# Optimization experiments

Measured on AMD Instinct MI355X. Metric: run time of the kernel, lower is better.

The kernel has to match this reference:

```python
import jax, jax.numpy as jnp
import numpy as np

B, S, H = 4, 2048, 1024
E, I, K = 8, 2048, 2


def setup_inputs() -> dict:
    key = jax.random.key(0)
    ks = jax.random.split(key, 6)
    return {
        "hidden_states": jax.random.normal(ks[0], (B, S, H), dtype=jnp.float32),
        "Wg": jax.random.normal(ks[1], (H, E), dtype=jnp.float32) * 0.02,
        "W1": jax.random.normal(ks[2], (E, H, I), dtype=jnp.float32) * 0.02,
        "b1": jnp.zeros((E, I), dtype=jnp.float32),
        "W2": jax.random.normal(ks[3], (E, I, H), dtype=jnp.float32) * 0.02,
        "b2": jnp.zeros((E, H), dtype=jnp.float32),
    }


def reference(hidden_states, Wg, W1, b1, W2, b2):
    b, s, h = hidden_states.shape
    x = hidden_states.reshape(-1, h)                      # [T, H]
    gate_logits = x @ Wg                                  # [T, E]
    gate_probs = jax.nn.softmax(gate_logits, axis=-1)
    topk_probs, topk_idx = jax.lax.top_k(gate_probs, K)   # [T, K]
    topk_probs = topk_probs / jnp.sum(topk_probs, axis=-1, keepdims=True)
    # dense combine weights [T, E] (zero where expert not selected)
    T = x.shape[0]
    w = jnp.zeros((T, E), dtype=x.dtype)
    w = w.at[jnp.arange(T)[:, None], topk_idx].set(topk_probs)
    # run every expert on all tokens (dense grouped-GEMM form), exact erf GELU
    h1 = jax.nn.gelu(jnp.einsum('th,ehi->eti', x, W1) + b1[:, None, :], approximate=False)  # [E, T, I]
    y = jnp.einsum('eti,eih->eth', h1, W2) + b2[:, None, :]                                  # [E, T, H]
    out = jnp.einsum('te,eth->th', w, y)                                                     # [T, H]
    return out.reshape(b, s, h)
```

## Files before the change

### kernel.cpp

```cpp
#include <hip/hip_runtime.h>
#include <math.h>

#define TOKS 8192
#define HD 1024
#define ID 2048
#define NE 8

typedef __bf16 bf16_t;
typedef __bf16 bf16x8 __attribute__((ext_vector_type(8)));
typedef float f32x4 __attribute__((ext_vector_type(4)));

#define GLOAD(gp, lp)                                                \
  __builtin_amdgcn_global_load_lds(                                  \
      (const __attribute__((address_space(1))) void*)(gp),           \
      (__attribute__((address_space(3))) void*)(lp), 16, 0, 0)

#define WAITV(N) asm volatile("s_waitcnt vmcnt(" #N ")" ::: "memory")
#define WAITL0() asm volatile("s_waitcnt lgkmcnt(0)" ::: "memory")

#define WS_COUNTS 0
#define WS_OFFSETS 32
#define WS_BTOK 128
#define WS_BW (128 + 65536)
#define WS_TE (128 + 2 * 65536)
#define WS_TW (128 + 3 * 65536)
#define WS_WL 263168ull
#define WS_BLKC 266240ull
#define WS_BLKB 270336ull
#define WS_XB 524288ull
#define WS_H1 (WS_XB + 16777216ull)
#define WS_WT (WS_H1 + 67108864ull)

#define MAXWL 144
#define BM 128

__global__ void zero_kernel(float* __restrict__ out) {
  const int i = (blockIdx.x * 256 + threadIdx.x) * 4;
  *(float4*)(out + i) = make_float4(0.f, 0.f, 0.f, 0.f);
}

__global__ void convert_kernel(const float* __restrict__ x, bf16_t* __restrict__ xb) {
  const size_t i = ((size_t)blockIdx.x * 256 + threadIdx.x) * 8;
  const float4 a = *(const float4*)(x + i);
  const float4 b = *(const float4*)(x + i + 4);
  bf16_t o[8] = {(bf16_t)a.x, (bf16_t)a.y, (bf16_t)a.z, (bf16_t)a.w,
                 (bf16_t)b.x, (bf16_t)b.y, (bf16_t)b.z, (bf16_t)b.w};
  *(uint4*)(xb + i) = *(uint4*)o;
}

__global__ __launch_bounds__(256) void gate_kernel(const float* __restrict__ x,
                                                   const float* __restrict__ Wg,
                                                   int* __restrict__ tok_e,
                                                   float* __restrict__ tok_w) {
  __shared__ float WgT[NE][HD];
  const int tid = threadIdx.x;
#pragma unroll
  for (int i = 0; i < NE * HD / 256; ++i) {
    const int idx = i * 256 + tid;
    WgT[idx & 7][idx >> 3] = Wg[idx];
  }
  __syncthreads();
  const int wv = tid >> 6;
  const int lane = tid & 63;
#pragma unroll
  for (int s = 0; s < 2; ++s) {
    const int t = blockIdx.x * 8 + wv * 2 + s;
    const float* xrow = x + (size_t)t * HD;
    float acc[NE];
#pragma unroll
    for (int e = 0; e < NE; ++e) acc[e] = 0.f;
#pragma unroll
    for (int i = 0; i < 16; ++i) {
      const int h = i * 64 + lane;
      const float xv = xrow[h];
#pragma unroll
      for (int e = 0; e < NE; ++e) acc[e] += xv * WgT[e][h];
    }
#pragma unroll
    for (int off = 32; off >= 1; off >>= 1) {
#pragma unroll
      for (int e = 0; e < NE; ++e) acc[e] += __shfl_xor(acc[e], off);
    }
    if (lane == 0) {
      int i1 = 0;
      float l1 = acc[0];
#pragma unroll
      for (int e = 1; e < NE; ++e)
        if (acc[e] > l1) { l1 = acc[e]; i1 = e; }
      int i2 = -1;
      float l2 = -3.4e38f;
#pragma unroll
      for (int e = 0; e < NE; ++e)
        if (e != i1 && acc[e] > l2) { l2 = acc[e]; i2 = e; }
      const float q = expf(l2 - l1);
      const float w1 = 1.f / (1.f + q);
      tok_e[2 * t] = i1;
      tok_e[2 * t + 1] = i2;
      tok_w[2 * t] = w1;
      tok_w[2 * t + 1] = q * w1;
    }
  }
}

__global__ __launch_bounds__(256) void hist_kernel(const int* __restrict__ tok_e,
                                                   int* __restrict__ blk_cnt) {
  __shared__ int wcnt[4][NE];
  const int tid = threadIdx.x;
  const int idx = blockIdx.x * 256 + tid;
  const int e = tok_e[idx];
  const int w = tid >> 6;
  const int lane = tid & 63;
#pragma unroll
  for (int e0 = 0; e0 < NE; ++e0) {
    const unsigned long long m = __ballot(e == e0);
    if (lane == 0) wcnt[w][e0] = __popcll(m);
  }
  __syncthreads();
  if (tid < NE)
    blk_cnt[blockIdx.x * NE + tid] =
        wcnt[0][tid] + wcnt[1][tid] + wcnt[2][tid] + wcnt[3][tid];
}

__global__ void scan_kernel(const int* __restrict__ blk_cnt, int* __restrict__ counts,
                            int* __restrict__ offsets, int* __restrict__ blk_base,
                            int* __restrict__ wl_e, int* __restrict__ wl_m,
                            int* __restrict__ n_work) {
  const int b = threadIdx.x;
  int c[NE], pre[NE], tot[NE];
#pragma unroll
  for (int e = 0; e < NE; ++e) c[e] = blk_cnt[b * NE + e];
#pragma unroll
  for (int e = 0; e < NE; ++e) {
    int v = c[e];
#pragma unroll
    for (int off = 1; off < 64; off <<= 1) {
      const int u = __shfl_up(v, off);
      if (b >= off) v += u;
    }
    pre[e] = v - c[e];
    tot[e] = __shfl(v, 63);
  }
  int off_[NE];
  int s = 0;
#pragma unroll
  for (int e = 0; e < NE; ++e) {
    off_[e] = s;
    s += tot[e];
  }
#pragma unroll
  for (int e = 0; e < NE; ++e) blk_base[b * NE + e] = off_[e] + pre[e];
  if (b == 0) {
    int idx = 0;
    for (int e = 0; e < NE; ++e) {
      counts[e] = tot[e];
      offsets[e] = off_[e];
      for (int m = 0; m < tot[e] && idx < MAXWL; m += BM) {
        wl_e[idx] = e;
        wl_m[idx] = m;
        ++idx;
      }
    }
    *n_work = idx;
  }
}

__global__ __launch_bounds__(256) void scatter_kernel(const int* __restrict__ tok_e,
                                                      const float* __restrict__ tok_w,
                                                      const int* __restrict__ blk_base,
                                                      int* __restrict__ bucket_tok,
                                                      float* __restrict__ bucket_w) {
  __shared__ int wcnt[4][NE];
  const int tid = threadIdx.x;
  const int idx = blockIdx.x * 256 + tid;
  const int e = tok_e[idx];
  const int w = tid >> 6;
  const int lane = tid & 63;
  unsigned long long mym = 0;
#pragma unroll
  for (int e0 = 0; e0 < NE; ++e0) {
    const unsigned long long m = __ballot(e == e0);
    if (lane == 0) wcnt[w][e0] = __popcll(m);
    if (e0 == e) mym = m;
  }
  __syncthreads();
  int base = blk_base[blockIdx.x * NE + e];
  for (int w2 = 0; w2 < w; ++w2) base += wcnt[w2][e];
  const int rank = __popcll(mym & ((1ull << lane) - 1ull));
  const int pos = base + rank;
  bucket_tok[pos] = idx >> 1;
  bucket_w[pos] = tok_w[idx];
}

__global__ __launch_bounds__(256) void transpose_convert_kernel(const float* __restrict__ src,
                                                                bf16_t* __restrict__ dst, int K,
                                                                int N) {
  __shared__ float tile[64][65];
  const int e = blockIdx.z;
  const int k0 = blockIdx.x * 64;
  const int n0 = blockIdx.y * 64;
  const float* s = src + (size_t)e * K * N;
  bf16_t* d = dst + (size_t)e * K * N;
  const int t = threadIdx.x;
  const int c = t & 63;
  const int r4 = t >> 6;
#pragma unroll
  for (int p = 0; p < 16; ++p) {
    const int r = p * 4 + r4;
    tile[r][c] = s[(size_t)(k0 + r) * N + n0 + c];
  }
  __syncthreads();
  const int kc = t & 7;
  const int nb = t >> 3;
#pragma unroll
  for (int p = 0; p < 2; ++p) {
    const int n = p * 32 + nb;
    bf16_t o[8];
#pragma unroll
    for (int j = 0; j < 8; ++j) o[j] = (bf16_t)tile[kc * 8 + j][n];
    *(uint4*)(d + (size_t)(n0 + n) * K + k0 + kc * 8) = *(uint4*)o;
  }
}


__global__ __launch_bounds__(256, 3) void gemm1_kernel(
    const bf16_t* __restrict__ xb, const bf16_t* __restrict__ W1T, const float* __restrict__ b1,
    const int* __restrict__ counts, const int* __restrict__ offsets,
    const int* __restrict__ bucket_tok, const int* __restrict__ wl_e,
    const int* __restrict__ wl_m, const int* __restrict__ n_work, bf16_t* __restrict__ h1) {
  const int widx = blockIdx.x;
  if (widx >= *n_work) return;
  const int e = wl_e[widx];
  const int m_base = wl_m[widx];
  const int n_e = counts[e];
  const int n_base = blockIdx.y * 128;
  const int off = offsets[e];

  __shared__ bf16_t As[3][128 * 32];
  __shared__ bf16_t Bs[3][128 * 32];

  const int tid = threadIdx.x;
  const int w = tid >> 6;
  const int lane = tid & 63;
  const int quad = lane >> 4;
  const int lrow = lane & 15;
  const int wm = w >> 1;
  const int wn = w & 1;

  const int srow = lane >> 2;
  const int kch = (((lane & 3) ^ (srow & 3)) * 8);
  int r0 = m_base + w * 32 + srow;
  int r1 = r0 + 16;
  if (r0 >= n_e) r0 = n_e - 1;
  if (r1 >= n_e) r1 = n_e - 1;
  const bf16_t* ga0 = xb + (size_t)bucket_tok[off + r0] * HD + kch;
  const bf16_t* ga1 = xb + (size_t)bucket_tok[off + r1] * HD + kch;
  const bf16_t* gb0 = W1T + ((size_t)e * ID + n_base + w * 32 + srow) * HD + kch;
  const bf16_t* gb1 = gb0 + (size_t)16 * HD;
  const int laofs0 = w * 1024 + lane * 8;
  const int laofs1 = laofs0 + 512;

  f32x4 acc[4][4];
#pragma unroll
  for (int mt = 0; mt < 4; ++mt)
#pragma unroll
    for (int nt = 0; nt < 4; ++nt)
#pragma unroll
      for (int r = 0; r < 4; ++r) acc[mt][nt][r] = 0.f;

#pragma unroll
  for (int p = 0; p < 2; ++p) {
    const size_t ko = (size_t)p * 32;
    GLOAD(ga0 + ko, &As[p][laofs0]);
    GLOAD(ga1 + ko, &As[p][laofs1]);
    GLOAD(gb0 + ko, &Bs[p][laofs0]);
    GLOAD(gb1 + ko, &Bs[p][laofs1]);
  }

#define NT1 (HD / 32)
  for (int kt = 0; kt < NT1; ++kt) {
    WAITL0();
    __builtin_amdgcn_s_barrier();
    if (kt + 2 < NT1) {
      const int nxt = (kt + 2) % 3;
      const size_t ko = (size_t)(kt + 2) * 32;
      GLOAD(ga0 + ko, &As[nxt][laofs0]);
      GLOAD(ga1 + ko, &As[nxt][laofs1]);
      GLOAD(gb0 + ko, &Bs[nxt][laofs0]);
      GLOAD(gb1 + ko, &Bs[nxt][laofs1]);
      WAITV(8);
    } else if (kt + 1 < NT1) {
      WAITV(4);
    } else {
      WAITV(0);
    }
    __builtin_amdgcn_s_barrier();
    __builtin_amdgcn_sched_barrier(0);
    const int cur = kt % 3;
    const int slot = (quad ^ (lrow & 3)) * 8;
    bf16x8 af[4], bfr[4];
#pragma unroll
    for (int i = 0; i < 4; ++i) {
      af[i] = *(const bf16x8*)(&As[cur][(wm * 64 + i * 16 + lrow) * 32 + slot]);
      bfr[i] = *(const bf16x8*)(&Bs[cur][(wn * 64 + i * 16 + lrow) * 32 + slot]);
    }
#pragma unroll
    for (int mt = 0; mt < 4; ++mt)
#pragma unroll
      for (int nt = 0; nt < 4; ++nt)
        acc[mt][nt] =
            __builtin_amdgcn_mfma_f32_16x16x32_bf16(af[mt], bfr[nt], acc[mt][nt], 0, 0, 0);
  }

#pragma unroll
  for (int mt = 0; mt < 4; ++mt) {
#pragma unroll
    for (int r = 0; r < 4; ++r) {
      const int gm = m_base + wm * 64 + mt * 16 + quad * 4 + r;
      if (gm < n_e) {
        bf16_t* orow = h1 + (size_t)(off + gm) * ID;
#pragma unroll
        for (int nt = 0; nt < 4; ++nt) {
          const int gi = n_base + wn * 64 + nt * 16 + lrow;
          float v = acc[mt][nt][r] + b1[e * ID + gi];
          v = 0.5f * v * (1.f + erff(v * 0.70710678118654752f));
          orow[gi] = (bf16_t)v;
        }
      }
    }
  }
}

__global__ __launch_bounds__(256, 3) void gemm2_kernel(
    const bf16_t* __restrict__ h1, const bf16_t* __restrict__ W2T, const float* __restrict__ b2,
    const int* __restrict__ counts, const int* __restrict__ offsets,
    const int* __restrict__ bucket_tok, const float* __restrict__ bucket_w,
    const int* __restrict__ wl_e, const int* __restrict__ wl_m, const int* __restrict__ n_work,
    float* __restrict__ out) {
  const int widx = blockIdx.x;
  if (widx >= *n_work) return;
  const int e = wl_e[widx];
  const int m_base = wl_m[widx];
  const int n_e = counts[e];
  const int n_base = blockIdx.y * 128;
  const int off = offsets[e];

  __shared__ bf16_t As[3][128 * 32];
  __shared__ bf16_t Bs[3][128 * 32];

  const int tid = threadIdx.x;
  const int w = tid >> 6;
  const int lane = tid & 63;
  const int quad = lane >> 4;
  const int lrow = lane & 15;
  const int wm = w >> 1;
  const int wn = w & 1;

  const int srow = lane >> 2;
  const int kch = (((lane & 3) ^ (srow & 3)) * 8);
  int r0 = m_base + w * 32 + srow;
  int r1 = r0 + 16;
  if (r0 >= n_e) r0 = n_e - 1;
  if (r1 >= n_e) r1 = n_e - 1;
  const bf16_t* ga0 = h1 + (size_t)(off + r0) * ID + kch;
  const bf16_t* ga1 = h1 + (size_t)(off + r1) * ID + kch;
  const bf16_t* gb0 = W2T + ((size_t)e * HD + n_base + w * 32 + srow) * ID + kch;
  const bf16_t* gb1 = gb0 + (size_t)16 * ID;
  const int laofs0 = w * 1024 + lane * 8;
  const int laofs1 = laofs0 + 512;

  f32x4 acc[4][4];
#pragma unroll
  for (int mt = 0; mt < 4; ++mt)
#pragma unroll
    for (int nt = 0; nt < 4; ++nt)
#pragma unroll
      for (int r = 0; r < 4; ++r) acc[mt][nt][r] = 0.f;

#pragma unroll
  for (int p = 0; p < 2; ++p) {
    const size_t ko = (size_t)p * 32;
    GLOAD(ga0 + ko, &As[p][laofs0]);
    GLOAD(ga1 + ko, &As[p][laofs1]);
    GLOAD(gb0 + ko, &Bs[p][laofs0]);
    GLOAD(gb1 + ko, &Bs[p][laofs1]);
  }

#define NT2 (ID / 32)
  for (int kt = 0; kt < NT2; ++kt) {
    WAITL0();
    __builtin_amdgcn_s_barrier();
    if (kt + 2 < NT2) {
      const int nxt = (kt + 2) % 3;
      const size_t ko = (size_t)(kt + 2) * 32;
      GLOAD(ga0 + ko, &As[nxt][laofs0]);
      GLOAD(ga1 + ko, &As[nxt][laofs1]);
      GLOAD(gb0 + ko, &Bs[nxt][laofs0]);
      GLOAD(gb1 + ko, &Bs[nxt][laofs1]);
      WAITV(8);
    } else if (kt + 1 < NT2) {
      WAITV(4);
    } else {
      WAITV(0);
    }
    __builtin_amdgcn_s_barrier();
    __builtin_amdgcn_sched_barrier(0);
    const int cur = kt % 3;
    const int slot = (quad ^ (lrow & 3)) * 8;
    bf16x8 af[4], bfr[4];
#pragma unroll
    for (int i = 0; i < 4; ++i) {
      af[i] = *(const bf16x8*)(&As[cur][(wm * 64 + i * 16 + lrow) * 32 + slot]);
      bfr[i] = *(const bf16x8*)(&Bs[cur][(wn * 64 + i * 16 + lrow) * 32 + slot]);
    }
#pragma unroll
    for (int mt = 0; mt < 4; ++mt)
#pragma unroll
      for (int nt = 0; nt < 4; ++nt)
        acc[mt][nt] =
            __builtin_amdgcn_mfma_f32_16x16x32_bf16(af[mt], bfr[nt], acc[mt][nt], 0, 0, 0);
  }

#pragma unroll
  for (int mt = 0; mt < 4; ++mt) {
#pragma unroll
    for (int r = 0; r < 4; ++r) {
      const int gm = m_base + wm * 64 + mt * 16 + quad * 4 + r;
      if (gm < n_e) {
        const int pos = off + gm;
        const int tokid = bucket_tok[pos];
        const float wgt = bucket_w[pos];
        float* orow = out + (size_t)tokid * HD;
#pragma unroll
        for (int nt = 0; nt < 4; ++nt) {
          const int gh = n_base + wn * 64 + nt * 16 + lrow;
          float v = acc[mt][nt][r] + b2[e * HD + gh];
          atomicAdd(orow + gh, wgt * v);
        }
      }
    }
  }
}

extern "C" void kernel_launch(void* const* d_in, const int* in_sizes, int n_in,
                              void* d_out, int out_size, void* d_ws, size_t ws_size,
                              hipStream_t stream) {
  const float* x = (const float*)d_in[0];
  const float* Wg = (const float*)d_in[1];
  const float* W1 = (const float*)d_in[2];
  const float* b1 = (const float*)d_in[3];
  const float* W2 = (const float*)d_in[4];
  const float* b2 = (const float*)d_in[5];
  float* out = (float*)d_out;
  char* ws = (char*)d_ws;

  int* counts = (int*)(ws + WS_COUNTS);
  int* offsets = (int*)(ws + WS_OFFSETS);
  int* bucket_tok = (int*)(ws + WS_BTOK);
  float* bucket_w = (float*)(ws + WS_BW);
  int* tok_e = (int*)(ws + WS_TE);
  float* tok_w = (float*)(ws + WS_TW);
  int* wl_e = (int*)(ws + WS_WL);
  int* wl_m = wl_e + MAXWL;
  int* n_work = wl_m + MAXWL;
  int* blk_cnt = (int*)(ws + WS_BLKC);
  int* blk_base = (int*)(ws + WS_BLKB);
  bf16_t* xb = (bf16_t*)(ws + WS_XB);
  bf16_t* h1 = (bf16_t*)(ws + WS_H1);
  bf16_t* WT = (bf16_t*)(ws + WS_WT);

  zero_kernel<<<(TOKS * HD / 4) / 256, 256, 0, stream>>>(out);
  convert_kernel<<<TOKS * HD / (256 * 8), 256, 0, stream>>>(x, xb);
  gate_kernel<<<TOKS / 8, 256, 0, stream>>>(x, Wg, tok_e, tok_w);
  hist_kernel<<<TOKS * 2 / 256, 256, 0, stream>>>(tok_e, blk_cnt);
  scan_kernel<<<1, 64, 0, stream>>>(blk_cnt, counts, offsets, blk_base, wl_e, wl_m, n_work);
  scatter_kernel<<<TOKS * 2 / 256, 256, 0, stream>>>(tok_e, tok_w, blk_base, bucket_tok,
                                                     bucket_w);
  transpose_convert_kernel<<<dim3(HD / 64, ID / 64, NE), 256, 0, stream>>>(W1, WT, HD, ID);
  gemm1_kernel<<<dim3(MAXWL, ID / 128), 256, 0, stream>>>(xb, WT, b1, counts, offsets, bucket_tok,
                                                          wl_e, wl_m, n_work, h1);
  transpose_convert_kernel<<<dim3(ID / 64, HD / 64, NE), 256, 0, stream>>>(W2, WT, ID, HD);
  gemm2_kernel<<<dim3(MAXWL, HD / 128), 256, 0, stream>>>(h1, WT, b2, counts, offsets,
                                                          bucket_tok, bucket_w, wl_e, wl_m,
                                                          n_work, out);
}
```

Baseline: 542.4 us.

## Enlarge grouped GEMM tiles to 256x128x64 with 512-thread double-buffered blocks

Both expert GEMMs move from 128x128 tiles with K-step 32 and a triple-buffered async pipeline to 256-row by 128-column tiles with K-step 64. They now use 8 waves per block, double buffering and plain __syncthreads. The LDS swizzle widens to 8 chunks and the work list shrinks to match the new row tile. The aim is more data reuse per block and fewer barriers per unit of K. In exchange, occupancy falls to one block per CU, only one stage is prefetched, and more rows may be wasted as padding per expert.

Result: slower. 648.6 us (+19.6%).

```diff
diff --git a/kernel.cpp b/kernel.cpp
--- a/kernel.cpp
+++ b/kernel.cpp
@@ -14,9 +14,6 @@
   __builtin_amdgcn_global_load_lds(                                  \
       (const __attribute__((address_space(1))) void*)(gp),           \
       (__attribute__((address_space(3))) void*)(lp), 16, 0, 0)
-
-#define WAITV(N) asm volatile("s_waitcnt vmcnt(" #N ")" ::: "memory")
-#define WAITL0() asm volatile("s_waitcnt lgkmcnt(0)" ::: "memory")
 
 #define WS_COUNTS 0
 #define WS_OFFSETS 32
@@ -31,8 +28,8 @@
 #define WS_H1 (WS_XB + 16777216ull)
 #define WS_WT (WS_H1 + 67108864ull)
 
-#define MAXWL 144
-#define BM 128
+#define MAXWL 80
+#define BM 256
 
 __global__ void zero_kernel(float* __restrict__ out) {
   const int i = (blockIdx.x * 256 + threadIdx.x) * 4;
@@ -222,7 +219,7 @@
 }
 
 
-__global__ __launch_bounds__(256, 3) void gemm1_kernel(
+__global__ __launch_bounds__(512, 1) void gemm1_kernel(
     const bf16_t* __restrict__ xb, const bf16_t* __restrict__ W1T, const float* __restrict__ b1,
     const int* __restrict__ counts, const int* __restrict__ offsets,
     const int* __restrict__ bucket_tok, const int* __restrict__ wl_e,
@@ -235,8 +232,8 @@
   const int n_base = blockIdx.y * 128;
   const int off = offsets[e];
 
-  __shared__ bf16_t As[3][128 * 32];
-  __shared__ bf16_t Bs[3][128 * 32];
+  __shared__ bf16_t As[2][256 * 64];
+  __shared__ bf16_t Bs[2][128 * 64];
 
   const int tid = threadIdx.x;
   const int w = tid >> 6;
@@ -246,18 +243,24 @@
   const int wm = w >> 1;
   const int wn = w & 1;
 
-  const int srow = lane >> 2;
-  const int kch = (((lane & 3) ^ (srow & 3)) * 8);
-  int r0 = m_base + w * 32 + srow;
-  int r1 = r0 + 16;
-  if (r0 >= n_e) r0 = n_e - 1;
-  if (r1 >= n_e) r1 = n_e - 1;
-  const bf16_t* ga0 = xb + (size_t)bucket_tok[off + r0] * HD + kch;
-  const bf16_t* ga1 = xb + (size_t)bucket_tok[off + r1] * HD + kch;
-  const bf16_t* gb0 = W1T + ((size_t)e * ID + n_base + w * 32 + srow) * HD + kch;
-  const bf16_t* gb1 = gb0 + (size_t)16 * HD;
-  const int laofs0 = w * 1024 + lane * 8;
-  const int laofs1 = laofs0 + 512;
+  const int srow = lane >> 3;
+  const int kch = (((lane & 7) ^ (srow & 7)) * 8);
+  const bf16_t* ga[4];
+#pragma unroll
+  for (int g = 0; g < 4; ++g) {
+    int r = m_base + w * 32 + g * 8 + srow;
+    if (r >= n_e) r = n_e - 1;
+    ga[g] = xb + (size_t)bucket_tok[off + r] * HD + kch;
+  }
+  const bf16_t* gb[2];
+#pragma unroll
+  for (int g = 0; g < 2; ++g)
+    gb[g] = W1T + ((size_t)e * ID + n_base + w * 16 + g * 8 + srow) * HD + kch;
+  int aofs[4], bofs[2];
+#pragma unroll
+  for (int g = 0; g < 4; ++g) aofs[g] = (w * 32 + g * 8) * 64 + lane * 8;
+#pragma unroll
+  for (int g = 0; g < 2; ++g) bofs[g] = (w * 16 + g * 8) * 64 + lane * 8;
 
   f32x4 acc[4][4];
 #pragma unroll
@@ -267,48 +270,43 @@
 #pragma unroll
       for (int r = 0; r < 4; ++r) acc[mt][nt][r] = 0.f;
 
-#pragma unroll
-  for (int p = 0; p < 2; ++p) {
-    const size_t ko = (size_t)p * 32;
-    GLOAD(ga0 + ko, &As[p][laofs0]);
-    GLOAD(ga1 + ko, &As[p][laofs1]);
-    GLOAD(gb0 + ko, &Bs[p][laofs0]);
-    GLOAD(gb1 + ko, &Bs[p][laofs1]);
-  }
-
-#define NT1 (HD / 32)
+  const int s0 = ((0 * 4 + quad) ^ (lrow & 7)) * 8;
+  const int s1 = ((1 * 4 + quad) ^ (lrow & 7)) * 8;
+
+#pragma unroll
+  for (int g = 0; g < 4; ++g) GLOAD(ga[g], &As[0][aofs[g]]);
+#pragma unroll
+  for (int g = 0; g < 2; ++g) GLOAD(gb[g], &Bs[0][bofs[g]]);
+  __syncthreads();
+
+#define NT1 (HD / 64)
   for (int kt = 0; kt < NT1; ++kt) {
-    WAITL0();
-    __builtin_amdgcn_s_barrier();
-    if (kt + 2 < NT1) {
-      const int nxt = (kt + 2) % 3;
-      const size_t ko = (size_t)(kt + 2) * 32;
-      GLOAD(ga0 + ko, &As[nxt][laofs0]);
-      GLOAD(ga1 + ko, &As[nxt][laofs1]);
-      GLOAD(gb0 + ko, &Bs[nxt][laofs0]);
-      GLOAD(gb1 + ko, &Bs[nxt][laofs1]);
-      WAITV(8);
-    } else if (kt + 1 < NT1) {
-      WAITV(4);
-    } else {
-      WAITV(0);
-    }
-    __builtin_amdgcn_s_barrier();
-    __builtin_amdgcn_sched_barrier(0);
-    const int cur = kt % 3;
-    const int slot = (quad ^ (lrow & 3)) * 8;
-    bf16x8 af[4], bfr[4];
-#pragma unroll
-    for (int i = 0; i < 4; ++i) {
-      af[i] = *(const bf16x8*)(&As[cur][(wm * 64 + i * 16 + lrow) * 32 + slot]);
-      bfr[i] = *(const bf16x8*)(&Bs[cur][(wn * 64 + i * 16 + lrow) * 32 + slot]);
-    }
-#pragma unroll
-    for (int mt = 0; mt < 4; ++mt)
-#pragma unroll
-      for (int nt = 0; nt < 4; ++nt)
-        acc[mt][nt] =
-            __builtin_amdgcn_mfma_f32_16x16x32_bf16(af[mt], bfr[nt], acc[mt][nt], 0, 0, 0);
+    const int cur = kt & 1;
+    if (kt + 1 < NT1) {
+      const int nxt = cur ^ 1;
+      const size_t ko = (size_t)(kt + 1) * 64;
+#pragma unroll
+      for (int g = 0; g < 4; ++g) GLOAD(ga[g] + ko, &As[nxt][aofs[g]]);
+#pragma unroll
+      for (int g = 0; g < 2; ++g) GLOAD(gb[g] + ko, &Bs[nxt][bofs[g]]);
+    }
+#pragma unroll
+    for (int kk = 0; kk < 2; ++kk) {
+      const int sl = kk ? s1 : s0;
+      bf16x8 af[4], bfr[4];
+#pragma unroll
+      for (int i = 0; i < 4; ++i) {
+        af[i] = *(const bf16x8*)(&As[cur][(wm * 64 + i * 16 + lrow) * 64 + sl]);
+        bfr[i] = *(const bf16x8*)(&Bs[cur][(wn * 64 + i * 16 + lrow) * 64 + sl]);
+      }
+#pragma unroll
+      for (int mt = 0; mt < 4; ++mt)
+#pragma unroll
+        for (int nt = 0; nt < 4; ++nt)
+          acc[mt][nt] =
+              __builtin_amdgcn_mfma_f32_16x16x32_bf16(af[mt], bfr[nt], acc[mt][nt], 0, 0, 0);
+    }
+    __syncthreads();
   }
 
 #pragma unroll
@@ -330,7 +328,7 @@
   }
 }
 
-__global__ __launch_bounds__(256, 3) void gemm2_kernel(
+__global__ __launch_bounds__(512, 1) void gemm2_kernel(
     const bf16_t* __restrict__ h1, const bf16_t* __restrict__ W2T, const float* __restrict__ b2,
     const int* __restrict__ counts, const int* __restrict__ offsets,
     const int* __restrict__ bucket_tok, const float* __restrict__ bucket_w,
@@ -344,8 +342,8 @@
   const int n_base = blockIdx.y * 128;
   const int off = offsets[e];
 
-  __shared__ bf16_t As[3][128 * 32];
-  __shared__ bf16_t Bs[3][128 * 32];
+  __shared__ bf16_t As[2][256 * 64];
+  __shared__ bf16_t Bs[2][128 * 64];
 
   const int tid = threadIdx.x;
   const int w = tid >> 6;
@@ -355,18 +353,24 @@
   const int wm = w >> 1;
   const int wn = w & 1;
 
-  const int srow = lane >> 2;
-  const int kch = (((lane & 3) ^ (srow & 3)) * 8);
-  int r0 = m_base + w * 32 + srow;
-  int r1 = r0 + 16;
-  if (r0 >= n_e) r0 = n_e - 1;
-  if (r1 >= n_e) r1 = n_e - 1;
-  const bf16_t* ga0 = h1 + (size_t)(off + r0) * ID + kch;
-  const bf16_t* ga1 = h1 + (size_t)(off + r1) * ID + kch;
-  const bf16_t* gb0 = W2T + ((size_t)e * HD + n_base + w * 32 + srow) * ID + kch;
-  const bf16_t* gb1 = gb0 + (size_t)16 * ID;
-  const int laofs0 = w * 1024 + lane * 8;
-  const int laofs1 = laofs0 + 512;
+  const int srow = lane >> 3;
+  const int kch = (((lane & 7) ^ (srow & 7)) * 8);
+  const bf16_t* ga[4];
+#pragma unroll
+  for (int g = 0; g < 4; ++g) {
+    int r = m_base + w * 32 + g * 8 + srow;
+    if (r >= n_e) r = n_e - 1;
+    ga[g] = h1 + (size_t)(off + r) * ID + kch;
+  }
+  const bf16_t* gb[2];
+#pragma unroll
+  for (int g = 0; g < 2; ++g)
+    gb[g] = W2T + ((size_t)e * HD + n_base + w * 16 + g * 8 + srow) * ID + kch;
+  int aofs[4], bofs[2];
+#pragma unroll
+  for (int g = 0; g < 4; ++g) aofs[g] = (w * 32 + g * 8) * 64 + lane * 8;
+#pragma unroll
+  for (int g = 0; g < 2; ++g) bofs[g] = (w * 16 + g * 8) * 64 + lane * 8;
 
   f32x4 acc[4][4];
 #pragma unroll
@@ -376,48 +380,43 @@
 #pragma unroll
       for (int r = 0; r < 4; ++r) acc[mt][nt][r] = 0.f;
 
-#pragma unroll
-  for (int p = 0; p < 2; ++p) {
-    const size_t ko = (size_t)p * 32;
-    GLOAD(ga0 + ko, &As[p][laofs0]);
-    GLOAD(ga1 + ko, &As[p][laofs1]);
-    GLOAD(gb0 + ko, &Bs[p][laofs0]);
-    GLOAD(gb1 + ko, &Bs[p][laofs1]);
-  }
-
-#define NT2 (ID / 32)
+  const int s0 = ((0 * 4 + quad) ^ (lrow & 7)) * 8;
+  const int s1 = ((1 * 4 + quad) ^ (lrow & 7)) * 8;
+
+#pragma unroll
+  for (int g = 0; g < 4; ++g) GLOAD(ga[g], &As[0][aofs[g]]);
+#pragma unroll
+  for (int g = 0; g < 2; ++g) GLOAD(gb[g], &Bs[0][bofs[g]]);
+  __syncthreads();
+
+#define NT2 (ID / 64)
   for (int kt = 0; kt < NT2; ++kt) {
-    WAITL0();
-    __builtin_amdgcn_s_barrier();
-    if (kt + 2 < NT2) {
-      const int nxt = (kt + 2) % 3;
-      const size_t ko = (size_t)(kt + 2) * 32;
-      GLOAD(ga0 + ko, &As[nxt][laofs0]);
-      GLOAD(ga1 + ko, &As[nxt][laofs1]);
-      GLOAD(gb0 + ko, &Bs[nxt][laofs0]);
-      GLOAD(gb1 + ko, &Bs[nxt][laofs1]);
-      WAITV(8);
-    } else if (kt + 1 < NT2) {
-      WAITV(4);
-    } else {
-      WAITV(0);
-    }
-    __builtin_amdgcn_s_barrier();
-    __builtin_amdgcn_sched_barrier(0);
-    const int cur = kt % 3;
-    const int slot = (quad ^ (lrow & 3)) * 8;
-    bf16x8 af[4], bfr[4];
-#pragma unroll
-    for (int i = 0; i < 4; ++i) {
-      af[i] = *(const bf16x8*)(&As[cur][(wm * 64 + i * 16 + lrow) * 32 + slot]);
-      bfr[i] = *(const bf16x8*)(&Bs[cur][(wn * 64 + i * 16 + lrow) * 32 + slot]);
-    }
-#pragma unroll
-    for (int mt = 0; mt < 4; ++mt)
-#pragma unroll
-      for (int nt = 0; nt < 4; ++nt)
-        acc[mt][nt] =
-            __builtin_amdgcn_mfma_f32_16x16x32_bf16(af[mt], bfr[nt], acc[mt][nt], 0, 0, 0);
+    const int cur = kt & 1;
+    if (kt + 1 < NT2) {
+      const int nxt = cur ^ 1;
+      const size_t ko = (size_t)(kt + 1) * 64;
+#pragma unroll
+      for (int g = 0; g < 4; ++g) GLOAD(ga[g] + ko, &As[nxt][aofs[g]]);
+#pragma unroll
+      for (int g = 0; g < 2; ++g) GLOAD(gb[g] + ko, &Bs[nxt][bofs[g]]);
+    }
+#pragma unroll
+    for (int kk = 0; kk < 2; ++kk) {
+      const int sl = kk ? s1 : s0;
+      bf16x8 af[4], bfr[4];
+#pragma unroll
+      for (int i = 0; i < 4; ++i) {
+        af[i] = *(const bf16x8*)(&As[cur][(wm * 64 + i * 16 + lrow) * 64 + sl]);
+        bfr[i] = *(const bf16x8*)(&Bs[cur][(wn * 64 + i * 16 + lrow) * 64 + sl]);
+      }
+#pragma unroll
+      for (int mt = 0; mt < 4; ++mt)
+#pragma unroll
+        for (int nt = 0; nt < 4; ++nt)
+          acc[mt][nt] =
+              __builtin_amdgcn_mfma_f32_16x16x32_bf16(af[mt], bfr[nt], acc[mt][nt], 0, 0, 0);
+    }
+    __syncthreads();
   }
 
 #pragma unroll
@@ -476,10 +475,10 @@
   scatter_kernel<<<TOKS * 2 / 256, 256, 0, stream>>>(tok_e, tok_w, blk_base, bucket_tok,
                                                      bucket_w);
   transpose_convert_kernel<<<dim3(HD / 64, ID / 64, NE), 256, 0, stream>>>(W1, WT, HD, ID);
-  gemm1_kernel<<<dim3(MAXWL, ID / 128), 256, 0, stream>>>(xb, WT, b1, counts, offsets, bucket_tok,
+  gemm1_kernel<<<dim3(MAXWL, ID / 128), 512, 0, stream>>>(xb, WT, b1, counts, offsets, bucket_tok,
                                                           wl_e, wl_m, n_work, h1);
   transpose_convert_kernel<<<dim3(ID / 64, HD / 64, NE), 256, 0, stream>>>(W2, WT, ID, HD);
-  gemm2_kernel<<<dim3(MAXWL, HD / 128), 256, 0, stream>>>(h1, WT, b2, counts, offsets,
+  gemm2_kernel<<<dim3(MAXWL, HD / 128), 512, 0, stream>>>(h1, WT, b2, counts, offsets,
                                                           bucket_tok, bucket_w, wl_e, wl_m,
                                                           n_work, out);
 }
```

## Replace atomic scatter-add in gemm2 with bf16 staging and a combine kernel

Applied to the files above, without the earlier changes.

gemm2 now writes per-slot expert outputs in bf16 to a staging buffer instead of doing weighted float atomicAdds into the output. A new combine kernel gathers each token's two expert rows through a position map from the scatter kernel and writes the weighted sum directly, so the zeroing kernel is no longer needed. This removes 16M atomic operations and the output memset, at the cost of an extra 32MB round trip and a bf16 rounding of the expert outputs.

Result: faster. 480.2 us (-11.5%).

```diff
diff --git a/kernel.cpp b/kernel.cpp
--- a/kernel.cpp
+++ b/kernel.cpp
@@ -27,17 +27,14 @@
 #define WS_WL 263168ull
 #define WS_BLKC 266240ull
 #define WS_BLKB 270336ull
+#define WS_POS 274432ull
 #define WS_XB 524288ull
 #define WS_H1 (WS_XB + 16777216ull)
 #define WS_WT (WS_H1 + 67108864ull)
+#define WS_Y (WS_WT + 33554432ull)
 
 #define MAXWL 144
 #define BM 128
-
-__global__ void zero_kernel(float* __restrict__ out) {
-  const int i = (blockIdx.x * 256 + threadIdx.x) * 4;
-  *(float4*)(out + i) = make_float4(0.f, 0.f, 0.f, 0.f);
-}
 
 __global__ void convert_kernel(const float* __restrict__ x, bf16_t* __restrict__ xb) {
   const size_t i = ((size_t)blockIdx.x * 256 + threadIdx.x) * 8;
@@ -168,7 +165,8 @@
                                                       const float* __restrict__ tok_w,
                                                       const int* __restrict__ blk_base,
                                                       int* __restrict__ bucket_tok,
-                                                      float* __restrict__ bucket_w) {
+                                                      float* __restrict__ bucket_w,
+                                                      int* __restrict__ pos_of) {
   __shared__ int wcnt[4][NE];
   const int tid = threadIdx.x;
   const int idx = blockIdx.x * 256 + tid;
@@ -189,6 +187,7 @@
   const int pos = base + rank;
   bucket_tok[pos] = idx >> 1;
   bucket_w[pos] = tok_w[idx];
+  pos_of[idx] = pos;
 }
 
 __global__ __launch_bounds__(256) void transpose_convert_kernel(const float* __restrict__ src,
@@ -333,9 +332,8 @@
 __global__ __launch_bounds__(256, 3) void gemm2_kernel(
     const bf16_t* __restrict__ h1, const bf16_t* __restrict__ W2T, const float* __restrict__ b2,
     const int* __restrict__ counts, const int* __restrict__ offsets,
-    const int* __restrict__ bucket_tok, const float* __restrict__ bucket_w,
     const int* __restrict__ wl_e, const int* __restrict__ wl_m, const int* __restrict__ n_work,
-    float* __restrict__ out) {
+    bf16_t* __restrict__ y) {
   const int widx = blockIdx.x;
   if (widx >= *n_work) return;
   const int e = wl_e[widx];
@@ -426,19 +424,33 @@
     for (int r = 0; r < 4; ++r) {
       const int gm = m_base + wm * 64 + mt * 16 + quad * 4 + r;
       if (gm < n_e) {
-        const int pos = off + gm;
-        const int tokid = bucket_tok[pos];
-        const float wgt = bucket_w[pos];
-        float* orow = out + (size_t)tokid * HD;
+        bf16_t* orow = y + (size_t)(off + gm) * HD;
 #pragma unroll
         for (int nt = 0; nt < 4; ++nt) {
           const int gh = n_base + wn * 64 + nt * 16 + lrow;
-          float v = acc[mt][nt][r] + b2[e * HD + gh];
-          atomicAdd(orow + gh, wgt * v);
+          orow[gh] = (bf16_t)(acc[mt][nt][r] + b2[e * HD + gh]);
         }
       }
     }
   }
+}
+
+__global__ __launch_bounds__(256) void combine_kernel(const bf16_t* __restrict__ y,
+                                                      const int* __restrict__ pos_of,
+                                                      const float* __restrict__ tok_w,
+                                                      float* __restrict__ out) {
+  const int gid = blockIdx.x * 256 + threadIdx.x;
+  const int t = gid >> 7;
+  const int c8 = (gid & 127) * 8;
+  const int p1 = pos_of[2 * t];
+  const int p2 = pos_of[2 * t + 1];
+  const float w1 = tok_w[2 * t];
+  const float w2 = tok_w[2 * t + 1];
+  const bf16x8 a = *(const bf16x8*)(y + (size_t)p1 * HD + c8);
+  const bf16x8 b = *(const bf16x8*)(y + (size_t)p2 * HD + c8);
+  float* op = out + (size_t)t * HD + c8;
+#pragma unroll
+  for (int j = 0; j < 8; ++j) op[j] = w1 * (float)a[j] + w2 * (float)b[j];
 }
 
 extern "C" void kernel_launch(void* const* d_in, const int* in_sizes, int n_in,
@@ -464,22 +476,23 @@
   int* n_work = wl_m + MAXWL;
   int* blk_cnt = (int*)(ws + WS_BLKC);
   int* blk_base = (int*)(ws + WS_BLKB);
+  int* pos_of = (int*)(ws + WS_POS);
   bf16_t* xb = (bf16_t*)(ws + WS_XB);
   bf16_t* h1 = (bf16_t*)(ws + WS_H1);
   bf16_t* WT = (bf16_t*)(ws + WS_WT);
-
-  zero_kernel<<<(TOKS * HD / 4) / 256, 256, 0, stream>>>(out);
+  bf16_t* y = (bf16_t*)(ws + WS_Y);
+
   convert_kernel<<<TOKS * HD / (256 * 8), 256, 0, stream>>>(x, xb);
   gate_kernel<<<TOKS / 8, 256, 0, stream>>>(x, Wg, tok_e, tok_w);
   hist_kernel<<<TOKS * 2 / 256, 256, 0, stream>>>(tok_e, blk_cnt);
   scan_kernel<<<1, 64, 0, stream>>>(blk_cnt, counts, offsets, blk_base, wl_e, wl_m, n_work);
   scatter_kernel<<<TOKS * 2 / 256, 256, 0, stream>>>(tok_e, tok_w, blk_base, bucket_tok,
-                                                     bucket_w);
+                                                     bucket_w, pos_of);
   transpose_convert_kernel<<<dim3(HD / 64, ID / 64, NE), 256, 0, stream>>>(W1, WT, HD, ID);
   gemm1_kernel<<<dim3(MAXWL, ID / 128), 256, 0, stream>>>(xb, WT, b1, counts, offsets, bucket_tok,
                                                           wl_e, wl_m, n_work, h1);
   transpose_convert_kernel<<<dim3(ID / 64, HD / 64, NE), 256, 0, stream>>>(W2, WT, ID, HD);
-  gemm2_kernel<<<dim3(MAXWL, HD / 128), 256, 0, stream>>>(h1, WT, b2, counts, offsets,
-                                                          bucket_tok, bucket_w, wl_e, wl_m,
-                                                          n_work, out);
-}
+  gemm2_kernel<<<dim3(MAXWL, HD / 128), 256, 0, stream>>>(h1, WT, b2, counts, offsets, wl_e,
+                                                          wl_m, n_work, y);
+  combine_kernel<<<TOKS * HD / (256 * 8), 256, 0, stream>>>(y, pos_of, tok_w, out);
+}
```
